# Optimization experiments

Measured on AMD Instinct MI355X. Metric: run time of the kernel, lower is better.

The kernel has to match this reference:

```python
import jax, jax.numpy as jnp
import numpy as np

B, N, K, IN_CH = 512, 64, 16, 6   # graphs, nodes per graph, knn, input features
EPS = 1e-5


def _w(key, shape, fan_in):
    return jax.random.normal(key, shape, jnp.float32) / np.sqrt(fan_in)


def setup_inputs() -> dict:
    key = jax.random.key(0)
    ks = jax.random.split(key, 16)
    f32 = jnp.float32
    inp = {
        "x": jax.random.normal(ks[0], (B * N, IN_CH), f32),
        "batch": (jnp.arange(B * N, dtype=jnp.int32) // N).astype(jnp.int32),
        # input projection 6 -> 64
        "w_in": _w(ks[1], (IN_CH, 64), IN_CH), "g_in": jnp.ones(64, f32), "b_in": jnp.zeros(64, f32),
        # ec1: SharedMLP([128, 64, 64])
        "w1a": _w(ks[2], (128, 64), 128), "g1a": jnp.ones(64, f32), "b1a": jnp.zeros(64, f32),
        "w1b": _w(ks[3], (64, 64), 64),   "g1b": jnp.ones(64, f32), "b1b": jnp.zeros(64, f32),
        # ec2: SharedMLP([128, 128, 128])
        "w2a": _w(ks[4], (128, 128), 128), "g2a": jnp.ones(128, f32), "b2a": jnp.zeros(128, f32),
        "w2b": _w(ks[5], (128, 128), 128), "g2b": jnp.ones(128, f32), "b2b": jnp.zeros(128, f32),
        # ec3: SharedMLP([256, 256, 256])
        "w3a": _w(ks[6], (256, 256), 256), "g3a": jnp.ones(256, f32), "b3a": jnp.zeros(256, f32),
        "w3b": _w(ks[7], (256, 256), 256), "g3b": jnp.ones(256, f32), "b3b": jnp.zeros(256, f32),
        # classifier head (dropout is identity in eval mode)
        "wc1": _w(ks[8], (896, 512), 896), "gc1": jnp.ones(512, f32), "bc1": jnp.zeros(512, f32),
        "wc2": _w(ks[9], (512, 256), 512), "gc2": jnp.ones(256, f32), "bc2": jnp.zeros(256, f32),
        "wc3": _w(ks[10], (256, 2), 256),  "bc3": jnp.zeros(2, f32),
    }
    return inp


def bn(h, g, b):
    # training-mode BatchNorm1d over all leading (node/edge) dims, biased var
    ax = tuple(range(h.ndim - 1))
    m = h.mean(ax)
    v = h.var(ax)
    return g * (h - m) * jax.lax.rsqrt(v + EPS) + b


def lrelu(h):
    return jax.nn.leaky_relu(h, 0.2)


def knn(x):
    # x: [B,N,C]; per-graph squared-Euclidean kNN (excluding self)
    sq = jnp.sum(x * x, -1)
    d = sq[:, :, None] - 2.0 * jnp.einsum('bnc,bmc->bnm', x, x) + sq[:, None, :]
    _, idx = jax.lax.top_k(-d, K + 1)  # K+1 smallest distances
    return idx[:, :, 1:]               # drop self -> [B,N,K]


def edge_conv(x, w1, g1, b1, w2, g2, b2):
    # Dynamic EdgeConv, aggr='max'. Edge (src=centre c, dst=neighbour n):
    # target x_i = x_n, message = MLP(cat[x_i, x_j - x_i]) with x_j = x_c.
    idx = knn(x)                                     # [B,N,K]
    xn = jax.vmap(lambda xb, ib: xb[ib])(x, idx)     # [B,N,K,C] neighbours
    xc = x[:, :, None, :]                            # centres broadcast
    feat = jnp.concatenate([xn, xc - xn], -1)        # [B,N,K,2C]
    h = lrelu(bn(feat @ w1, g1, b1))
    h = lrelu(bn(h @ w2, g2, b2))                    # [B,N,K,Cout]
    C = h.shape[-1]

    def scatter_max(ib, hb):  # per-graph max-scatter to destination nodes
        out = jnp.full((N, C), -jnp.inf, hb.dtype)
        return out.at[ib.reshape(-1)].max(hb.reshape(-1, C))

    res = jax.vmap(scatter_max)(idx, h)
    return jnp.where(jnp.isneginf(res), 0.0, res)    # nodes w/o in-edges -> 0


def reference(x, batch, w_in, g_in, b_in,
              w1a, g1a, b1a, w1b, g1b, b1b,
              w2a, g2a, b2a, w2b, g2b, b2b,
              w3a, g3a, b3a, w3b, g3b, b3b,
              wc1, gc1, bc1, wc2, gc2, bc2, wc3, bc3):
    # batch == arange(B*N)//N (equal-size graphs), encoded by the [B,N] reshape
    h0 = lrelu(bn(x @ w_in, g_in, b_in)).reshape(B, N, 64)
    h1 = edge_conv(h0, w1a, g1a, b1a, w1b, g1b, b1b)   # [B,N,64]
    h2 = edge_conv(h1, w2a, g2a, b2a, w2b, g2b, b2b)   # [B,N,128]
    h3 = edge_conv(h2, w3a, g3a, b3a, w3b, g3b, b3b)   # [B,N,256]
    h = jnp.concatenate([h1, h2, h3], -1)              # [B,N,448]
    pooled = jnp.concatenate([h.mean(1), h.max(1)], -1)  # [B,896]
    z = lrelu(bn(pooled @ wc1, gc1, bc1))
    z = lrelu(bn(z @ wc2, gc2, bc2))
    return z @ wc3 + bc3                               # [B,2] logits
```

## Files before the change

kernel.cpp:

```cpp
#include <hip/hip_runtime.h>
#include <hip/hip_fp16.h>
#include <math.h>

#define BB 512
#define NN 64
#define KNB 16
#define NPTS (BB*NN)
#define NEDGE (BB*NN*KNB)
#define EPSV 1e-5f

typedef __attribute__((ext_vector_type(8))) _Float16 f16x8;
typedef __attribute__((ext_vector_type(4))) _Float16 f16x4;
typedef __attribute__((ext_vector_type(4))) float f32x4;

__device__ __forceinline__ float lrelu(float x){ return x > 0.0f ? x : 0.2f*x; }
__device__ __forceinline__ unsigned encf(float f){
    unsigned u = __float_as_uint(f);
    return (u & 0x80000000u) ? ~u : (u | 0x80000000u);
}
__device__ __forceinline__ float decf(unsigned e){
    unsigned u = (e & 0x80000000u) ? (e ^ 0x80000000u) : ~e;
    return __uint_as_float(u);
}
#define ENC_NEGINF 0x007FFFFFu

__device__ __forceinline__ void split2h(float v, _Float16& h, _Float16& m){
    h = (_Float16)v;
    float r = v - (float)h;
    m = (_Float16)(r * 2048.0f);
}

__global__ void k_input(const float* __restrict__ x, const float* __restrict__ w,
                        float* __restrict__ h0){
    __shared__ float wls[6*64];
    int t = threadIdx.x;
    for (int i = t; i < 6*64; i += 256) wls[i] = w[i];
    __syncthreads();
    int row = blockIdx.x*256 + t;
    float xv[6];
#pragma unroll
    for (int k = 0; k < 6; k++) xv[k] = x[row*6 + k];
#pragma unroll 8
    for (int c = 0; c < 64; c++){
        float acc = 0.f;
#pragma unroll
        for (int k = 0; k < 6; k++) acc += xv[k]*wls[k*64 + c];
        h0[(size_t)row*64 + c] = acc;
    }
}

__global__ void k_colstats_part(const float* __restrict__ h,
                                float* __restrict__ pS, float* __restrict__ pQ){
    int t = threadIdx.x;
    int c = t & 63;
    int g = t >> 6;
    int p = blockIdx.x*4 + g;
    const int rpb = NPTS/256;
    int r0 = p*rpb;
    float s = 0.f, q = 0.f;
    for (int r = r0; r < r0 + rpb; r++){
        float v = h[(size_t)r*64 + c];
        s += v; q += v*v;
    }
    pS[c*256 + p] = s;
    pQ[c*256 + p] = q;
}

__global__ void k_bnfin_part(const float* __restrict__ pS, const float* __restrict__ pQ,
                             const float* __restrict__ g, const float* __restrict__ b,
                             float* __restrict__ cA, float* __restrict__ cB,
                             int P, float invM){
    int c = threadIdx.x;
    const float* ps = pS + (size_t)c*P;
    const float* pq = pQ + (size_t)c*P;
    float s = 0.f, q = 0.f;
    for (int p = 0; p < P; p += 4){
        float4 vs = *(const float4*)(ps + p);
        float4 vq = *(const float4*)(pq + p);
        s += vs.x + vs.y + vs.z + vs.w;
        q += vq.x + vq.y + vq.z + vq.w;
    }
    float m = s*invM;
    float v = q*invM - m*m;
    v = v < 0.f ? 0.f : v;
    float a = g[c]*rsqrtf(v + EPSV);
    cA[c] = a;
    cB[c] = b[c] - m*a;
}

__global__ void k_bnfin(const float* gs, const float* gq, const float* g,
                        const float* b, float* cA, float* cB, int C, float invM){
    int c = blockIdx.x*blockDim.x + threadIdx.x;
    if (c < C){
        float m = gs[c]*invM;
        float v = gq[c]*invM - m*m;
        v = v < 0.f ? 0.f : v;
        float a = g[c]*rsqrtf(v + EPSV);
        cA[c] = a;
        cB[c] = b[c] - m*a;
    }
}

__global__ void k_apply(float* h, const float* __restrict__ cA,
                        const float* __restrict__ cB, int C, int total){
    int i = blockIdx.x*256 + threadIdx.x;
    if (i < total){
        int c = i & (C-1);
        h[i] = lrelu(cA[c]*h[i] + cB[c]);
    }
}

template<int C>
__global__ void k_knn(const float* __restrict__ x, int* __restrict__ idxg){
    const int CP = C + 4;
    __shared__ __align__(16) float xls[64*CP];
    __shared__ float sq[64];
    __shared__ __align__(16) float dls[64*64];
    int t = threadIdx.x, b = blockIdx.x;
    const float* xb = x + (size_t)b*64*C;
    for (int i = t; i < 64*C; i += 256){
        int n = i / C, c = i & (C-1);
        xls[n*CP + c] = xb[i];
    }
    __syncthreads();
    if (t < 64){
        float s = 0.f;
        for (int c = 0; c < C; c += 4){
            float4 v = *(const float4*)&xls[t*CP + c];
            s += v.x*v.x + v.y*v.y + v.z*v.z + v.w*v.w;
        }
        sq[t] = s;
    }
    __syncthreads();
    {
        int n  = t >> 2;
        int m0 = (t & 3)*16;
        float acc[16];
#pragma unroll
        for (int i = 0; i < 16; i++) acc[i] = 0.f;
        const float* an = &xls[n*CP];
        const float* bm = &xls[m0*CP];
        for (int c = 0; c < C; c += 4){
            float4 a = *(const float4*)(an + c);
#pragma unroll
            for (int i = 0; i < 16; i++){
                float4 bv = *(const float4*)(bm + i*CP + c);
                acc[i] += a.x*bv.x + a.y*bv.y + a.z*bv.z + a.w*bv.w;
            }
        }
        float sn = sq[n];
#pragma unroll
        for (int i4 = 0; i4 < 16; i4 += 4){
            float4 dv;
            dv.x = sn - 2.0f*acc[i4+0] + sq[m0+i4+0];
            dv.y = sn - 2.0f*acc[i4+1] + sq[m0+i4+1];
            dv.z = sn - 2.0f*acc[i4+2] + sq[m0+i4+2];
            dv.w = sn - 2.0f*acc[i4+3] + sq[m0+i4+3];
            *(float4*)&dls[n*64 + m0 + i4] = dv;
        }
    }
    __syncthreads();
    int lane = t & 63, w = t >> 6;
    for (int pr = 0; pr < 16; pr += 4){
        int n0 = w*16 + pr;
        unsigned long long c0 = (((unsigned long long)encf(dls[(n0+0)*64 + lane])) << 32) | (unsigned)lane;
        unsigned long long c1 = (((unsigned long long)encf(dls[(n0+1)*64 + lane])) << 32) | (unsigned)lane;
        unsigned long long c2 = (((unsigned long long)encf(dls[(n0+2)*64 + lane])) << 32) | (unsigned)lane;
        unsigned long long c3 = (((unsigned long long)encf(dls[(n0+3)*64 + lane])) << 32) | (unsigned)lane;
#pragma unroll
        for (int k = 2; k <= 64; k <<= 1){
#pragma unroll
            for (int j = k >> 1; j > 0; j >>= 1){
                bool keepmin = ((lane & j) == 0) == ((lane & k) == 0);
                unsigned long long o0 = __shfl_xor(c0, j, 64);
                unsigned long long o1 = __shfl_xor(c1, j, 64);
                unsigned long long o2 = __shfl_xor(c2, j, 64);
                unsigned long long o3 = __shfl_xor(c3, j, 64);
                c0 = keepmin ? (c0 < o0 ? c0 : o0) : (c0 < o0 ? o0 : c0);
                c1 = keepmin ? (c1 < o1 ? c1 : o1) : (c1 < o1 ? o1 : c1);
                c2 = keepmin ? (c2 < o2 ? c2 : o2) : (c2 < o2 ? o2 : c2);
                c3 = keepmin ? (c3 < o3 ? c3 : o3) : (c3 < o3 ? o3 : c3);
            }
        }
        if (lane >= 1 && lane <= KNB){
            int base = b*1024 + n0*16 + lane - 1;
            idxg[base]      = (int)(c0 & 0xffffffffu);
            idxg[base + 16] = (int)(c1 & 0xffffffffu);
            idxg[base + 32] = (int)(c2 & 0xffffffffu);
            idxg[base + 48] = (int)(c3 & 0xffffffffu);
        }
    }
}

template<int CIN, int CMID, bool SPLIT>
__global__ void k_wprep(const float* __restrict__ w1,
                        _Float16* __restrict__ wbh, _Float16* __restrict__ wbm,
                        _Float16* __restrict__ wdh, _Float16* __restrict__ wdm){
    int i = blockIdx.x*256 + threadIdx.x;
    if (i >= CIN*CMID) return;
    int k = i / CMID, c = i - k*CMID;
    float wb = w1[(size_t)(CIN + k)*CMID + c];
    float wd = w1[(size_t)k*CMID + c] - wb;
    size_t o = (size_t)c*CIN + k;
    if (SPLIT){
        _Float16 h, m;
        split2h(wb, h, m); wbh[o] = h; wbm[o] = m;
        split2h(wd, h, m); wdh[o] = h; wdm[o] = m;
    } else {
        wbh[o] = (_Float16)wb;
        wdh[o] = (_Float16)wd;
    }
}

template<int CIN, int CMID>
__global__ __launch_bounds__(256)
void k_mm1x(const float* __restrict__ x,
            const _Float16* __restrict__ wbh, const _Float16* __restrict__ wbm,
            const _Float16* __restrict__ wdh, const _Float16* __restrict__ wdm,
            float* __restrict__ P, float* __restrict__ Q){
    int t = threadIdx.x, b = blockIdx.x;
    int lane = t & 63, w = t >> 6;
    int lrow = lane & 15, lk = lane >> 4;
    const int KT = CIN/32;
    f16x8 ah[KT], am[KT];
    {
        const float* xr = x + ((size_t)b*64 + w*16 + lrow)*CIN;
#pragma unroll
        for (int kt = 0; kt < KT; kt++){
            union { f16x8 v; _Float16 u[8]; } H, M;
#pragma unroll
            for (int j = 0; j < 8; j++)
                split2h(xr[kt*32 + lk*8 + j], H.u[j], M.u[j]);
            ah[kt] = H.v; am[kt] = M.v;
        }
    }
#pragma unroll
    for (int ct = 0; ct < CMID/16; ct++){
        int col = ct*16 + lrow;
        f32x4 aPM = {0,0,0,0}, aPC = {0,0,0,0};
        f32x4 aQM = {0,0,0,0}, aQC = {0,0,0,0};
#pragma unroll
        for (int kt = 0; kt < KT; kt++){
            size_t bo = (size_t)col*CIN + kt*32 + lk*8;
            f16x8 bbh = *(const f16x8*)(wbh + bo);
            f16x8 bbm = *(const f16x8*)(wbm + bo);
            f16x8 bdh = *(const f16x8*)(wdh + bo);
            f16x8 bdm = *(const f16x8*)(wdm + bo);
            aPM = __builtin_amdgcn_mfma_f32_16x16x32_f16(ah[kt], bbh, aPM, 0, 0, 0);
            aPC = __builtin_amdgcn_mfma_f32_16x16x32_f16(ah[kt], bbm, aPC, 0, 0, 0);
            aPC = __builtin_amdgcn_mfma_f32_16x16x32_f16(am[kt], bbh, aPC, 0, 0, 0);
            aQM = __builtin_amdgcn_mfma_f32_16x16x32_f16(ah[kt], bdh, aQM, 0, 0, 0);
            aQC = __builtin_amdgcn_mfma_f32_16x16x32_f16(ah[kt], bdm, aQC, 0, 0, 0);
            aQC = __builtin_amdgcn_mfma_f32_16x16x32_f16(am[kt], bdh, aQC, 0, 0, 0);
        }
#pragma unroll
        for (int u = 0; u < 4; u++){
            size_t o = ((size_t)b*64 + w*16 + lk*4 + u)*CMID + col;
            P[o] = aPM[u] + aPC[u]*(1.0f/2048.0f);
            Q[o] = aQM[u] + aQC[u]*(1.0f/2048.0f);
        }
    }
}

template<int CIN, int CMID>
__global__ __launch_bounds__(256)
void k_mm1xh(const float* __restrict__ x,
             const _Float16* __restrict__ wbh, const _Float16* __restrict__ wdh,
             _Float16* __restrict__ P, _Float16* __restrict__ Q){
    int t = threadIdx.x, b = blockIdx.x;
    int lane = t & 63, w = t >> 6;
    int lrow = lane & 15, lk = lane >> 4;
    const int KT = CIN/32;
    f16x8 ah[KT];
    {
        const float* xr = x + ((size_t)b*64 + w*16 + lrow)*CIN;
#pragma unroll
        for (int kt = 0; kt < KT; kt++){
            union { f16x8 v; _Float16 u[8]; } H;
#pragma unroll
            for (int j = 0; j < 8; j++)
                H.u[j] = (_Float16)xr[kt*32 + lk*8 + j];
            ah[kt] = H.v;
        }
    }
#pragma unroll
    for (int ct = 0; ct < CMID/16; ct++){
        int col = ct*16 + lrow;
        f32x4 aP = {0,0,0,0}, aQ = {0,0,0,0};
#pragma unroll
        for (int kt = 0; kt < KT; kt++){
            size_t bo = (size_t)col*CIN + kt*32 + lk*8;
            f16x8 bbh = *(const f16x8*)(wbh + bo);
            f16x8 bdh = *(const f16x8*)(wdh + bo);
            aP = __builtin_amdgcn_mfma_f32_16x16x32_f16(ah[kt], bbh, aP, 0, 0, 0);
            aQ = __builtin_amdgcn_mfma_f32_16x16x32_f16(ah[kt], bdh, aQ, 0, 0, 0);
        }
#pragma unroll
        for (int u = 0; u < 4; u++){
            size_t o = ((size_t)b*64 + w*16 + lk*4 + u)*CMID + col;
            P[o] = (_Float16)aP[u];
            Q[o] = (_Float16)aQ[u];
        }
    }
}

template<int CMID>
__global__ void k_stats1p(const float* __restrict__ P, const float* __restrict__ Q,
                          const int* __restrict__ idxg,
                          float* __restrict__ pS, float* __restrict__ pQ){
    int t = threadIdx.x, b = blockIdx.x;
    const int NG = 256/CMID;
    const int PT = 512*NG;
    int c = t & (CMID-1);
    int g = t / CMID;
    int epg = 1024/NG;
    const float* Pb = P + (size_t)b*64*CMID;
    const float* Qb = Q + (size_t)b*64*CMID;
    const int* ib = idxg + b*1024;
    float s = 0.f, q = 0.f;
    for (int e = g*epg; e < (g+1)*epg; e++){
        int n = e >> 4;
        int j = ib[e];
        float v = Pb[n*CMID + c] + Qb[j*CMID + c];
        s += v; q += v*v;
    }
    int p = b*NG + g;
    pS[(size_t)c*PT + p] = s;
    pQ[(size_t)c*PT + p] = q;
}

__global__ void k_stats1h(const _Float16* __restrict__ P, const _Float16* __restrict__ Q,
                          const int* __restrict__ idxg,
                          float* __restrict__ pS, float* __restrict__ pQ){
    __shared__ int ils[1024];
    int t = threadIdx.x, b = blockIdx.x;
    for (int i = t; i < 1024; i += 256) ils[i] = idxg[b*1024 + i];
    __syncthreads();
    const _Float16* Pb = P + (size_t)b*64*256;
    const _Float16* Qb = Q + (size_t)b*64*256;
    float s = 0.f, q = 0.f;
    for (int n = 0; n < 64; n++){
        float p = (float)Pb[n*256 + t];
#pragma unroll 4
        for (int k = 0; k < 16; k++){
            int j = ils[n*16 + k];
            float v = p + (float)Qb[j*256 + t];
            s += v; q += v*v;
        }
    }
    pS[(size_t)t*512 + b] = s;
    pQ[(size_t)t*512 + b] = q;
}

template<int CMID, int COUT, int NSET>
__global__ __launch_bounds__(256)
void k_mm2s(const float* __restrict__ P, const float* __restrict__ Q,
            const int* __restrict__ idxg,
            const float* __restrict__ cA1, const float* __restrict__ cB1,
            const float* __restrict__ w2, const float* __restrict__ g2,
            unsigned* __restrict__ outenc,
            float* __restrict__ pS, float* __restrict__ pQ){
    const int AS = CMID + 8;
    const int NCOL = 64*NSET;
    __shared__ __align__(16) _Float16 act_h[32*AS];
    __shared__ __align__(16) _Float16 act_m[32*AS];
    __shared__ unsigned maxtab[NCOL*65];
    __shared__ int ils[1024];
    __shared__ __align__(16) float a1ls[CMID];
    __shared__ __align__(16) float b1ls[CMID];
    int t = threadIdx.x, b = blockIdx.x, cc = blockIdx.y;
    int lane = t & 63, w = t >> 6;
    int lrow = lane & 15, lk = lane >> 4;

    for (int i = t; i < 1024; i += 256) ils[i] = idxg[b*1024 + i];
    for (int i = t; i < CMID; i += 256){ a1ls[i] = cA1[i]; b1ls[i] = cB1[i]; }
    for (int i = t; i < NCOL*65; i += 256) maxtab[i] = ENC_NEGINF;

    const int KT = CMID/32;
    f16x8 bh[NSET][KT], bm[NSET][KT];
    float sg[NSET];
    int ccBase = cc*NCOL;
#pragma unroll
    for (int s = 0; s < NSET; s++){
        int ncol = ccBase + s*64 + w*16 + lrow;
#pragma unroll
        for (int kt = 0; kt < KT; kt++){
            union { f16x8 v; _Float16 u[8]; } uh, um;
#pragma unroll
            for (int j = 0; j < 8; j++){
                int k = kt*32 + lk*8 + j;
                split2h(w2[(size_t)k*COUT + ncol], uh.u[j], um.u[j]);
            }
            bh[s][kt] = uh.v; bm[s][kt] = um.v;
        }
        sg[s] = (g2[ncol] < 0.0f) ? -1.0f : 1.0f;
    }
    float ss[NSET], qq[NSET];
#pragma unroll
    for (int s = 0; s < NSET; s++){ ss[s] = 0.f; qq[s] = 0.f; }
    const float* Pb = P + (size_t)b*64*CMID;
    const float* Qb = Q + (size_t)b*64*CMID;
    __syncthreads();

    for (int ch = 0; ch < 32; ch++){
        for (int i = t*4; i < 32*CMID; i += 1024){
            int le = i / CMID, k = i & (CMID-1);
            int e = ch*32 + le;
            int n = e >> 4, j = ils[e];
            float4 pv = *(const float4*)(Pb + n*CMID + k);
            float4 qv = *(const float4*)(Qb + j*CMID + k);
            float4 ca = *(const float4*)&a1ls[k];
            float4 cb = *(const float4*)&b1ls[k];
            float v0 = lrelu(ca.x*(pv.x + qv.x) + cb.x);
            float v1 = lrelu(ca.y*(pv.y + qv.y) + cb.y);
            float v2 = lrelu(ca.z*(pv.z + qv.z) + cb.z);
            float v3 = lrelu(ca.w*(pv.w + qv.w) + cb.w);
            union { f16x4 v; _Float16 u[4]; } hh, mm;
            split2h(v0, hh.u[0], mm.u[0]);
            split2h(v1, hh.u[1], mm.u[1]);
            split2h(v2, hh.u[2], mm.u[2]);
            split2h(v3, hh.u[3], mm.u[3]);
            *(f16x4*)&act_h[le*AS + k] = hh.v;
            *(f16x4*)&act_m[le*AS + k] = mm.v;
        }
        __syncthreads();

        f32x4 accM[2][NSET], accC[2][NSET];
#pragma unroll
        for (int r = 0; r < 2; r++)
#pragma unroll
            for (int s = 0; s < NSET; s++){
                accM[r][s] = {0.f,0.f,0.f,0.f};
                accC[r][s] = {0.f,0.f,0.f,0.f};
            }
#pragma unroll
        for (int kt = 0; kt < KT; kt++){
            int ko = kt*32 + lk*8;
#pragma unroll
            for (int r = 0; r < 2; r++){
                f16x8 ah = *(const f16x8*)&act_h[(r*16 + lrow)*AS + ko];
                f16x8 am = *(const f16x8*)&act_m[(r*16 + lrow)*AS + ko];
#pragma unroll
                for (int s = 0; s < NSET; s++){
                    accM[r][s] = __builtin_amdgcn_mfma_f32_16x16x32_f16(ah, bh[s][kt], accM[r][s], 0, 0, 0);
                    accC[r][s] = __builtin_amdgcn_mfma_f32_16x16x32_f16(ah, bm[s][kt], accC[r][s], 0, 0, 0);
                    accC[r][s] = __builtin_amdgcn_mfma_f32_16x16x32_f16(am, bh[s][kt], accC[r][s], 0, 0, 0);
                }
            }
        }
#pragma unroll
        for (int r = 0; r < 2; r++){
#pragma unroll
            for (int s = 0; s < NSET; s++){
#pragma unroll
                for (int u = 0; u < 4; u++){
                    int e = ch*32 + r*16 + lk*4 + u;
                    float v = accM[r][s][u] + accC[r][s][u]*(1.0f/2048.0f);
                    ss[s] += v; qq[s] += v*v;
                    int colL = s*64 + w*16 + lrow;
                    atomicMax(&maxtab[colL*65 + ils[e]], encf(sg[s]*v));
                }
            }
        }
        __syncthreads();
    }
#pragma unroll
    for (int s = 0; s < NSET; s++){
        ss[s] += __shfl_xor(ss[s], 16, 64); ss[s] += __shfl_xor(ss[s], 32, 64);
        qq[s] += __shfl_xor(qq[s], 16, 64); qq[s] += __shfl_xor(qq[s], 32, 64);
        if (lane < 16){
            pS[(size_t)(ccBase + s*64 + w*16 + lane)*512 + b] = ss[s];
            pQ[(size_t)(ccBase + s*64 + w*16 + lane)*512 + b] = qq[s];
        }
    }
    for (int i = t; i < 64*NCOL; i += 256){
        int colL = i % NCOL, j = i / NCOL;
        outenc[((size_t)b*64 + j)*COUT + ccBase + colL] = maxtab[colL*65 + j];
    }
}

template<int CMID, int COUT, int NSET>
__global__ __launch_bounds__(256)
void k_mm2xh(const _Float16* __restrict__ P, const _Float16* __restrict__ Q,
             const int* __restrict__ idxg,
             const float* __restrict__ cA1, const float* __restrict__ cB1,
             const float* __restrict__ w2, const float* __restrict__ g2,
             unsigned* __restrict__ outenc,
             float* __restrict__ pS, float* __restrict__ pQ){
    const int AS = CMID + 8;
    const int NCOL = 64*NSET;
    __shared__ __align__(16) _Float16 act[32*AS];
    __shared__ unsigned maxtab[NCOL*65];
    __shared__ int ils[1024];
    __shared__ __align__(16) _Float16 a1h[CMID];
    __shared__ __align__(16) _Float16 b1h[CMID];
    int t = threadIdx.x, b = blockIdx.x, cc = blockIdx.y;
    int lane = t & 63, w = t >> 6;
    int lrow = lane & 15, lk = lane >> 4;

    for (int i = t; i < 1024; i += 256) ils[i] = idxg[b*1024 + i];
    for (int i = t; i < CMID; i += 256){
        a1h[i] = (_Float16)cA1[i];
        b1h[i] = (_Float16)cB1[i];
    }
    for (int i = t; i < NCOL*65; i += 256) maxtab[i] = ENC_NEGINF;

    const int KT = CMID/32;
    f16x8 breg[NSET][KT];
    float sg[NSET];
    int ccBase = cc*NCOL;
#pragma unroll
    for (int s = 0; s < NSET; s++){
        int ncol = ccBase + s*64 + w*16 + lrow;
#pragma unroll
        for (int kt = 0; kt < KT; kt++){
            union { f16x8 v; _Float16 u[8]; } bu;
#pragma unroll
            for (int j = 0; j < 8; j++){
                int k = kt*32 + lk*8 + j;
                bu.u[j] = (_Float16)w2[(size_t)k*COUT + ncol];
            }
            breg[s][kt] = bu.v;
        }
        sg[s] = (g2[ncol] < 0.0f) ? -1.0f : 1.0f;
    }
    float ss[NSET], qq[NSET];
#pragma unroll
    for (int s = 0; s < NSET; s++){ ss[s] = 0.f; qq[s] = 0.f; }
    const _Float16* Pb = P + (size_t)b*64*CMID;
    const _Float16* Qb = Q + (size_t)b*64*CMID;
    __syncthreads();

    for (int ch = 0; ch < 32; ch++){
        for (int i = t*8; i < 32*CMID; i += 2048){
            int le = i / CMID, k = i & (CMID-1);
            int e = ch*32 + le;
            int n = e >> 4, j = ils[e];
            f16x8 pv = *(const f16x8*)(Pb + (size_t)n*CMID + k);
            f16x8 qv = *(const f16x8*)(Qb + (size_t)j*CMID + k);
            f16x8 ca = *(const f16x8*)&a1h[k];
            f16x8 cb = *(const f16x8*)&b1h[k];
            f16x8 v = ca*(pv + qv) + cb;
            f16x8 vm = v * (_Float16)0.2f;
            union { f16x8 x; _Float16 e8[8]; } V, M, R;
            V.x = v; M.x = vm;
#pragma unroll
            for (int u = 0; u < 8; u++)
                R.e8[u] = (V.e8[u] > (_Float16)0.0f) ? V.e8[u] : M.e8[u];
            *(f16x8*)&act[le*AS + k] = R.x;
        }
        __syncthreads();

        f32x4 acc[2][NSET];
#pragma unroll
        for (int r = 0; r < 2; r++)
#pragma unroll
            for (int s = 0; s < NSET; s++) acc[r][s] = {0.f,0.f,0.f,0.f};
#pragma unroll
        for (int kt = 0; kt < KT; kt++){
            int ko = kt*32 + lk*8;
#pragma unroll
            for (int r = 0; r < 2; r++){
                f16x8 a = *(const f16x8*)&act[(r*16 + lrow)*AS + ko];
#pragma unroll
                for (int s = 0; s < NSET; s++)
                    acc[r][s] = __builtin_amdgcn_mfma_f32_16x16x32_f16(a, breg[s][kt], acc[r][s], 0, 0, 0);
            }
        }
#pragma unroll
        for (int r = 0; r < 2; r++){
#pragma unroll
            for (int s = 0; s < NSET; s++){
#pragma unroll
                for (int u = 0; u < 4; u++){
                    int e = ch*32 + r*16 + lk*4 + u;
                    float v = acc[r][s][u];
                    ss[s] += v; qq[s] += v*v;
                    int colL = s*64 + w*16 + lrow;
                    atomicMax(&maxtab[colL*65 + ils[e]], encf(sg[s]*v));
                }
            }
        }
        __syncthreads();
    }
#pragma unroll
    for (int s = 0; s < NSET; s++){
        ss[s] += __shfl_xor(ss[s], 16, 64); ss[s] += __shfl_xor(ss[s], 32, 64);
        qq[s] += __shfl_xor(qq[s], 16, 64); qq[s] += __shfl_xor(qq[s], 32, 64);
        if (lane < 16){
            pS[(size_t)(ccBase + s*64 + w*16 + lane)*512 + b] = ss[s];
            pQ[(size_t)(ccBase + s*64 + w*16 + lane)*512 + b] = qq[s];
        }
    }
    for (int i = t; i < 64*NCOL; i += 256){
        int colL = i % NCOL, j = i / NCOL;
        outenc[((size_t)b*64 + j)*COUT + ccBase + colL] = maxtab[colL*65 + j];
    }
}

__global__ void k_final_ec(unsigned* __restrict__ buf, const float* __restrict__ cA,
                           const float* __restrict__ cB, const float* __restrict__ g,
                           int C, int total){
    int i = blockIdx.x*256 + threadIdx.x;
    if (i >= total) return;
    int c = i & (C-1);
    unsigned e = buf[i];
    float r;
    if (e == ENC_NEGINF) r = 0.0f;
    else {
        float s = (g[c] < 0.0f) ? -1.0f : 1.0f;
        float v = s*decf(e);
        r = lrelu(cA[c]*v + cB[c]);
    }
    ((float*)buf)[i] = r;
}

__global__ void k_pool(const float* __restrict__ h1, const float* __restrict__ h2,
                       const unsigned* __restrict__ h3e,
                       const float* __restrict__ cA3, const float* __restrict__ cB3,
                       const float* __restrict__ g3, float* __restrict__ pooled){
    int t = threadIdx.x, b = blockIdx.x;
    for (int c = t; c < 448; c += 256){
        float s = 0.f, mx = -INFINITY;
        if (c < 192){
            const float* src; int C, cl;
            if (c < 64){ src = h1; C = 64;  cl = c; }
            else { src = h2; C = 128; cl = c - 64; }
            const float* p = src + (size_t)b*64*C + cl;
            for (int n = 0; n < 64; n++){
                float v = p[(size_t)n*C];
                s += v; mx = fmaxf(mx, v);
            }
        } else {
            int cl = c - 192;
            float ca = cA3[cl], cb = cB3[cl];
            float sgn = (g3[cl] < 0.0f) ? -1.0f : 1.0f;
            const unsigned* p = h3e + (size_t)b*64*256 + cl;
            for (int n = 0; n < 64; n++){
                unsigned e = p[(size_t)n*256];
                float v;
                if (e == ENC_NEGINF) v = 0.0f;
                else v = lrelu(ca*(sgn*decf(e)) + cb);
                s += v; mx = fmaxf(mx, v);
            }
        }
        pooled[b*896 + c] = s*(1.0f/64.0f);
        pooled[b*896 + 448 + c] = mx;
    }
}

__global__ void k_fc1(const float* __restrict__ pooled, const float* __restrict__ w,
                      float* __restrict__ z, float* gs, float* gq){
    int r = blockIdx.x;
    int co = blockIdx.y*256 + threadIdx.x;
    const float* pr = pooled + r*896;
    float acc = 0.f;
    for (int k = 0; k < 896; k++) acc += pr[k]*w[(size_t)k*512 + co];
    z[(size_t)r*512 + co] = acc;
    atomicAdd(&gs[co], acc);
    atomicAdd(&gq[co], acc*acc);
}

__global__ void k_fc2(const float* __restrict__ z1, const float* __restrict__ cA,
                      const float* __restrict__ cB, const float* __restrict__ w,
                      float* __restrict__ z2, float* gs, float* gq){
    int r = blockIdx.x;
    int co = threadIdx.x;
    const float* zr = z1 + (size_t)r*512;
    float acc = 0.f;
    for (int k = 0; k < 512; k++){
        float v = lrelu(cA[k]*zr[k] + cB[k]);
        acc += v*w[(size_t)k*256 + co];
    }
    z2[(size_t)r*256 + co] = acc;
    atomicAdd(&gs[co], acc);
    atomicAdd(&gq[co], acc*acc);
}

__global__ void k_fc3(const float* __restrict__ z2, const float* __restrict__ cA,
                      const float* __restrict__ cB, const float* __restrict__ w,
                      const float* __restrict__ bias, float* __restrict__ out){
    int r = blockIdx.x*256 + threadIdx.x;
    const float* zr = z2 + (size_t)r*256;
    float a0 = 0.f, a1 = 0.f;
    for (int k = 0; k < 256; k++){
        float v = lrelu(cA[k]*zr[k] + cB[k]);
        a0 += v*w[k*2 + 0];
        a1 += v*w[k*2 + 1];
    }
    out[r*2 + 0] = a0 + bias[0];
    out[r*2 + 1] = a1 + bias[1];
}

extern "C" void kernel_launch(void* const* d_in, const int* in_sizes, int n_in,
                              void* d_out, int out_size, void* d_ws, size_t ws_size,
                              hipStream_t stream){
    const float* x    = (const float*)d_in[0];
    const float* w_in = (const float*)d_in[2];
    const float* g_in = (const float*)d_in[3];
    const float* b_in = (const float*)d_in[4];
    const float* w1a  = (const float*)d_in[5];
    const float* g1a  = (const float*)d_in[6];
    const float* b1a  = (const float*)d_in[7];
    const float* w1b  = (const float*)d_in[8];
    const float* g1b  = (const float*)d_in[9];
    const float* b1b  = (const float*)d_in[10];
    const float* w2a  = (const float*)d_in[11];
    const float* g2a  = (const float*)d_in[12];
    const float* b2a  = (const float*)d_in[13];
    const float* w2b  = (const float*)d_in[14];
    const float* g2b  = (const float*)d_in[15];
    const float* b2b  = (const float*)d_in[16];
    const float* w3a  = (const float*)d_in[17];
    const float* g3a  = (const float*)d_in[18];
    const float* b3a  = (const float*)d_in[19];
    const float* w3b  = (const float*)d_in[20];
    const float* g3b  = (const float*)d_in[21];
    const float* b3b  = (const float*)d_in[22];
    const float* wc1  = (const float*)d_in[23];
    const float* gc1  = (const float*)d_in[24];
    const float* bc1  = (const float*)d_in[25];
    const float* wc2  = (const float*)d_in[26];
    const float* gc2  = (const float*)d_in[27];
    const float* bc2  = (const float*)d_in[28];
    const float* wc3  = (const float*)d_in[29];
    const float* bc3  = (const float*)d_in[30];

    char* ws = (char*)d_ws;
    size_t off = 0;
    auto alloc = [&](size_t bytes){
        size_t o = off; off = (off + bytes + 255) & ~(size_t)255; return o;
    };
    float* h0     = (float*)(ws + alloc((size_t)NPTS*64*4));
    float* h1     = (float*)(ws + alloc((size_t)NPTS*64*4));
    float* h2     = (float*)(ws + alloc((size_t)NPTS*128*4));
    float* h3     = (float*)(ws + alloc((size_t)NPTS*256*4));
    float* P      = (float*)(ws + alloc((size_t)NPTS*256*4));
    float* Q      = (float*)(ws + alloc((size_t)NPTS*256*4));
    int*   idx    = (int*)  (ws + alloc((size_t)NPTS*16*4));
    float* pooled = (float*)(ws + alloc((size_t)512*896*4));
    float* z1     = (float*)(ws + alloc((size_t)512*512*4));
    float* z2     = (float*)(ws + alloc((size_t)512*256*4));
    float* pS     = (float*)(ws + alloc((size_t)131072*4));
    float* pQ     = (float*)(ws + alloc((size_t)131072*4));
    float* stats  = (float*)(ws + alloc((size_t)2048*4));
    float* coefs  = (float*)(ws + alloc((size_t)3456*4));
    _Float16* wsp = (_Float16*)(ws + alloc((size_t)114688*2));

    _Float16 *w1bh = wsp,          *w1bm = wsp+4096,
             *w1dh = wsp+8192,     *w1dm = wsp+12288;
    _Float16 *w2bh = wsp+16384,    *w2bm = wsp+24576,
             *w2dh = wsp+32768,    *w2dm = wsp+40960;
    _Float16 *w3bh = wsp+49152,    *w3dh = wsp+81920;

    float *f1s  = stats,       *f1q  = stats+512;
    float *f2s  = stats+1024,  *f2q  = stats+1280;
    float *cA0   = coefs,      *cB0   = coefs+64;
    float *cA1a  = coefs+128,  *cB1a  = coefs+192;
    float *cA1b  = coefs+256,  *cB1b  = coefs+320;
    float *cA2a  = coefs+384,  *cB2a  = coefs+512;
    float *cA2b  = coefs+640,  *cB2b  = coefs+768;
    float *cA3a  = coefs+896,  *cB3a  = coefs+1152;
    float *cA3b  = coefs+1408, *cB3b  = coefs+1664;
    float *cAf1  = coefs+1920, *cBf1  = coefs+2432;
    float *cAf2  = coefs+2944, *cBf2  = coefs+3200;

    (void)hipMemsetAsync(stats, 0, 2048*4, stream);

    k_wprep<64,64,true><<<16, 256, 0, stream>>>(w1a, w1bh, w1bm, w1dh, w1dm);
    k_wprep<64,128,true><<<32, 256, 0, stream>>>(w2a, w2bh, w2bm, w2dh, w2dm);
    k_wprep<128,256,false><<<128, 256, 0, stream>>>(w3a, w3bh, nullptr, w3dh, nullptr);

    k_input<<<NPTS/256, 256, 0, stream>>>(x, w_in, h0);
    k_colstats_part<<<64, 256, 0, stream>>>(h0, pS, pQ);
    k_bnfin_part<<<1, 64, 0, stream>>>(pS, pQ, g_in, b_in, cA0, cB0, 256, 1.0f/NPTS);
    k_apply<<<(NPTS*64)/256, 256, 0, stream>>>(h0, cA0, cB0, 64, NPTS*64);

    k_knn<64><<<BB, 256, 0, stream>>>(h0, idx);
    k_mm1x<64,64><<<BB, 256, 0, stream>>>(h0, w1bh, w1bm, w1dh, w1dm, P, Q);
    k_stats1p<64><<<BB, 256, 0, stream>>>(P, Q, idx, pS, pQ);
    k_bnfin_part<<<1, 64, 0, stream>>>(pS, pQ, g1a, b1a, cA1a, cB1a, 2048, 1.0f/NEDGE);
    k_mm2s<64,64,1><<<dim3(BB,1), 256, 0, stream>>>(P, Q, idx, cA1a, cB1a, w1b, g1b,
                                                    (unsigned*)h1, pS, pQ);
    k_bnfin_part<<<1, 64, 0, stream>>>(pS, pQ, g1b, b1b, cA1b, cB1b, 512, 1.0f/NEDGE);
    k_final_ec<<<(NPTS*64)/256, 256, 0, stream>>>((unsigned*)h1, cA1b, cB1b, g1b, 64, NPTS*64);

    k_knn<64><<<BB, 256, 0, stream>>>(h1, idx);
    k_mm1x<64,128><<<BB, 256, 0, stream>>>(h1, w2bh, w2bm, w2dh, w2dm, P, Q);
    k_stats1p<128><<<BB, 256, 0, stream>>>(P, Q, idx, pS, pQ);
    k_bnfin_part<<<1, 128, 0, stream>>>(pS, pQ, g2a, b2a, cA2a, cB2a, 1024, 1.0f/NEDGE);
    k_mm2s<128,128,2><<<dim3(BB,1), 256, 0, stream>>>(P, Q, idx, cA2a, cB2a, w2b, g2b,
                                                      (unsigned*)h2, pS, pQ);
    k_bnfin_part<<<1, 128, 0, stream>>>(pS, pQ, g2b, b2b, cA2b, cB2b, 512, 1.0f/NEDGE);
    k_final_ec<<<(NPTS*128)/256, 256, 0, stream>>>((unsigned*)h2, cA2b, cB2b, g2b, 128, NPTS*128);

    k_knn<128><<<BB, 256, 0, stream>>>(h2, idx);
    k_mm1xh<128,256><<<BB, 256, 0, stream>>>(h2, w3bh, w3dh, (_Float16*)P, (_Float16*)Q);
    k_stats1h<<<BB, 256, 0, stream>>>((_Float16*)P, (_Float16*)Q, idx, pS, pQ);
    k_bnfin_part<<<1, 256, 0, stream>>>(pS, pQ, g3a, b3a, cA3a, cB3a, 512, 1.0f/NEDGE);
    k_mm2xh<256,256,2><<<dim3(BB,2), 256, 0, stream>>>((_Float16*)P, (_Float16*)Q, idx,
                                                       cA3a, cB3a, w3b, g3b,
                                                       (unsigned*)h3, pS, pQ);
    k_bnfin_part<<<1, 256, 0, stream>>>(pS, pQ, g3b, b3b, cA3b, cB3b, 512, 1.0f/NEDGE);

    k_pool<<<BB, 256, 0, stream>>>(h1, h2, (const unsigned*)h3, cA3b, cB3b, g3b, pooled);
    k_fc1<<<dim3(512,2), 256, 0, stream>>>(pooled, wc1, z1, f1s, f1q);
    k_bnfin<<<2, 256, 0, stream>>>(f1s, f1q, gc1, bc1, cAf1, cBf1, 512, 1.0f/512);
    k_fc2<<<512, 256, 0, stream>>>(z1, cAf1, cBf1, wc2, z2, f2s, f2q);
    k_bnfin<<<1, 256, 0, stream>>>(f2s, f2q, gc2, bc2, cAf2, cBf2, 256, 1.0f/512);
    k_fc3<<<2, 256, 0, stream>>>(z2, cAf2, cBf2, wc3, bc3, (float*)d_out);

    (void)in_sizes; (void)n_in; (void)out_size; (void)ws_size;
}
```

Before: 1.243 ms.

## Prefetch next chunk's gathered P/Q into registers and shrink shared index table

In both edge-MLP second-layer kernels, the P/Q gather loads for the next 32-edge chunk are issued into registers right after the barrier, so global latency overlaps the MFMA and atomic-max work of the current chunk. The neighbour index table is stored as bytes in shared memory, and the BN scale/shift constants are held in registers instead of shared arrays. Launch bounds now request 3 blocks per SM, and lrelu becomes an fmax. Extra prefetch registers combined with the tighter occupancy bound may cause register spills.

```diff
diff --git a/kernel.cpp b/kernel.cpp
--- a/kernel.cpp
+++ b/kernel.cpp
@@ -13,7 +13,7 @@
 typedef __attribute__((ext_vector_type(4))) _Float16 f16x4;
 typedef __attribute__((ext_vector_type(4))) float f32x4;
 
-__device__ __forceinline__ float lrelu(float x){ return x > 0.0f ? x : 0.2f*x; }
+__device__ __forceinline__ float lrelu(float x){ return fmaxf(x, 0.2f*x); }
 __device__ __forceinline__ unsigned encf(float f){
     unsigned u = __float_as_uint(f);
     return (u & 0x80000000u) ? ~u : (u | 0x80000000u);
@@ -353,7 +353,7 @@
 }
 
 template<int CMID, int COUT, int NSET>
-__global__ __launch_bounds__(256)
+__global__ __launch_bounds__(256, 3)
 void k_mm2s(const float* __restrict__ P, const float* __restrict__ Q,
             const int* __restrict__ idxg,
             const float* __restrict__ cA1, const float* __restrict__ cB1,
@@ -362,19 +362,23 @@
             float* __restrict__ pS, float* __restrict__ pQ){
     const int AS = CMID + 8;
     const int NCOL = 64*NSET;
+    const int NM = CMID/32;
+    const int LESTEP = 1024/CMID;
     __shared__ __align__(16) _Float16 act_h[32*AS];
     __shared__ __align__(16) _Float16 act_m[32*AS];
     __shared__ unsigned maxtab[NCOL*65];
-    __shared__ int ils[1024];
-    __shared__ __align__(16) float a1ls[CMID];
-    __shared__ __align__(16) float b1ls[CMID];
+    __shared__ unsigned char ils8[1024];
     int t = threadIdx.x, b = blockIdx.x, cc = blockIdx.y;
     int lane = t & 63, w = t >> 6;
     int lrow = lane & 15, lk = lane >> 4;
 
-    for (int i = t; i < 1024; i += 256) ils[i] = idxg[b*1024 + i];
-    for (int i = t; i < CMID; i += 256){ a1ls[i] = cA1[i]; b1ls[i] = cB1[i]; }
+    for (int i = t; i < 1024; i += 256) ils8[i] = (unsigned char)idxg[b*1024 + i];
     for (int i = t; i < NCOL*65; i += 256) maxtab[i] = ENC_NEGINF;
+
+    int kq  = (t*4) & (CMID-1);
+    int le0 = (t*4) / CMID;
+    float4 caq = *(const float4*)(cA1 + kq);
+    float4 cbq = *(const float4*)(cB1 + kq);
 
     const int KT = CMID/32;
     f16x8 bh[NSET][KT], bm[NSET][KT];
@@ -402,28 +406,49 @@
     const float* Qb = Q + (size_t)b*64*CMID;
     __syncthreads();
 
+    float4 pvr[NM], qvr[NM];
+#pragma unroll
+    for (int m = 0; m < NM; m++){
+        int le = le0 + LESTEP*m;
+        int j = ils8[le];
+        pvr[m] = *(const float4*)(Pb + (le >> 4)*CMID + kq);
+        qvr[m] = *(const float4*)(Qb + (size_t)j*CMID + kq);
+    }
+
     for (int ch = 0; ch < 32; ch++){
-        for (int i = t*4; i < 32*CMID; i += 1024){
-            int le = i / CMID, k = i & (CMID-1);
-            int e = ch*32 + le;
-            int n = e >> 4, j = ils[e];
-            float4 pv = *(const float4*)(Pb + n*CMID + k);
-            float4 qv = *(const float4*)(Qb + j*CMID + k);
-            float4 ca = *(const float4*)&a1ls[k];
-            float4 cb = *(const float4*)&b1ls[k];
-            float v0 = lrelu(ca.x*(pv.x + qv.x) + cb.x);
-            float v1 = lrelu(ca.y*(pv.y + qv.y) + cb.y);
-            float v2 = lrelu(ca.z*(pv.z + qv.z) + cb.z);
-            float v3 = lrelu(ca.w*(pv.w + qv.w) + cb.w);
+#pragma unroll
+        for (int m = 0; m < NM; m++){
+            int le = le0 + LESTEP*m;
+            float4 pv = pvr[m], qv = qvr[m];
+            float v0 = lrelu(caq.x*(pv.x + qv.x) + cbq.x);
+            float v1 = lrelu(caq.y*(pv.y + qv.y) + cbq.y);
+            float v2 = lrelu(caq.z*(pv.z + qv.z) + cbq.z);
+            float v3 = lrelu(caq.w*(pv.w + qv.w) + cbq.w);
             union { f16x4 v; _Float16 u[4]; } hh, mm;
             split2h(v0, hh.u[0], mm.u[0]);
             split2h(v1, hh.u[1], mm.u[1]);
             split2h(v2, hh.u[2], mm.u[2]);
             split2h(v3, hh.u[3], mm.u[3]);
-            *(f16x4*)&act_h[le*AS + k] = hh.v;
-            *(f16x4*)&act_m[le*AS + k] = mm.v;
+            *(f16x4*)&act_h[le*AS + kq] = hh.v;
+            *(f16x4*)&act_m[le*AS + kq] = mm.v;
         }
         __syncthreads();
+
+        if (ch < 31){
+#pragma unroll
+            for (int m = 0; m < NM; m++){
+                int le = le0 + LESTEP*m;
+                int j = ils8[(ch+1)*32 + le];
+                pvr[m] = *(const float4*)(Pb + ((ch+1)*2 + (le >> 4))*CMID + kq);
+                qvr[m] = *(const float4*)(Qb + (size_t)j*CMID + kq);
+            }
+        }
+        int jj[2][4];
+#pragma unroll
+        for (int r = 0; r < 2; r++)
+#pragma unroll
+            for (int u = 0; u < 4; u++)
+                jj[r][u] = ils8[ch*32 + r*16 + lk*4 + u];
 
         f32x4 accM[2][NSET], accC[2][NSET];
 #pragma unroll
@@ -454,11 +479,10 @@
             for (int s = 0; s < NSET; s++){
 #pragma unroll
                 for (int u = 0; u < 4; u++){
-                    int e = ch*32 + r*16 + lk*4 + u;
                     float v = accM[r][s][u] + accC[r][s][u]*(1.0f/2048.0f);
                     ss[s] += v; qq[s] += v*v;
                     int colL = s*64 + w*16 + lrow;
-                    atomicMax(&maxtab[colL*65 + ils[e]], encf(sg[s]*v));
+                    atomicMax(&maxtab[colL*65 + jj[r][u]], encf(sg[s]*v));
                 }
             }
         }
@@ -480,7 +504,7 @@
 }
 
 template<int CMID, int COUT, int NSET>
-__global__ __launch_bounds__(256)
+__global__ __launch_bounds__(256, 3)
 void k_mm2xh(const _Float16* __restrict__ P, const _Float16* __restrict__ Q,
              const int* __restrict__ idxg,
              const float* __restrict__ cA1, const float* __restrict__ cB1,
@@ -489,21 +513,26 @@
              float* __restrict__ pS, float* __restrict__ pQ){
     const int AS = CMID + 8;
     const int NCOL = 64*NSET;
+    const int NM = CMID/64;
+    const int LESTEP = 2048/CMID;
     __shared__ __align__(16) _Float16 act[32*AS];
     __shared__ unsigned maxtab[NCOL*65];
-    __shared__ int ils[1024];
-    __shared__ __align__(16) _Float16 a1h[CMID];
-    __shared__ __align__(16) _Float16 b1h[CMID];
+    __shared__ unsigned char ils8[1024];
     int t = threadIdx.x, b = blockIdx.x, cc = blockIdx.y;
     int lane = t & 63, w = t >> 6;
     int lrow = lane & 15, lk = lane >> 4;
 
-    for (int i = t; i < 1024; i += 256) ils[i] = idxg[b*1024 + i];
-    for (int i = t; i < CMID; i += 256){
-        a1h[i] = (_Float16)cA1[i];
-        b1h[i] = (_Float16)cB1[i];
-    }
+    for (int i = t; i < 1024; i += 256) ils8[i] = (unsigned char)idxg[b*1024 + i];
     for (int i = t; i < NCOL*65; i += 256) maxtab[i] = ENC_NEGINF;
+
+    int kq  = (t*8) & (CMID-1);
+    int le0 = (t*8) / CMID;
+    union { f16x8 v; _Float16 u[8]; } cah, cbh;
+#pragma unroll
+    for (int j = 0; j < 8; j++){
+        cah.u[j] = (_Float16)cA1[kq + j];
+        cbh.u[j] = (_Float16)cB1[kq + j];
+    }
 
     const int KT = CMID/32;
     f16x8 breg[NSET][KT];
@@ -531,25 +560,45 @@
     const _Float16* Qb = Q + (size_t)b*64*CMID;
     __syncthreads();
 
+    f16x8 pvr[NM], qvr[NM];
+#pragma unroll
+    for (int m = 0; m < NM; m++){
+        int le = le0 + LESTEP*m;
+        int j = ils8[le];
+        pvr[m] = *(const f16x8*)(Pb + (size_t)(le >> 4)*CMID + kq);
+        qvr[m] = *(const f16x8*)(Qb + (size_t)j*CMID + kq);
+    }
+
     for (int ch = 0; ch < 32; ch++){
-        for (int i = t*8; i < 32*CMID; i += 2048){
-            int le = i / CMID, k = i & (CMID-1);
-            int e = ch*32 + le;
-            int n = e >> 4, j = ils[e];
-            f16x8 pv = *(const f16x8*)(Pb + (size_t)n*CMID + k);
-            f16x8 qv = *(const f16x8*)(Qb + (size_t)j*CMID + k);
-            f16x8 ca = *(const f16x8*)&a1h[k];
-            f16x8 cb = *(const f16x8*)&b1h[k];
-            f16x8 v = ca*(pv + qv) + cb;
+#pragma unroll
+        for (int m = 0; m < NM; m++){
+            int le = le0 + LESTEP*m;
+            f16x8 v = cah.v*(pvr[m] + qvr[m]) + cbh.v;
             f16x8 vm = v * (_Float16)0.2f;
             union { f16x8 x; _Float16 e8[8]; } V, M, R;
             V.x = v; M.x = vm;
 #pragma unroll
             for (int u = 0; u < 8; u++)
                 R.e8[u] = (V.e8[u] > (_Float16)0.0f) ? V.e8[u] : M.e8[u];
-            *(f16x8*)&act[le*AS + k] = R.x;
+            *(f16x8*)&act[le*AS + kq] = R.x;
         }
         __syncthreads();
+
+        if (ch < 31){
+#pragma unroll
+            for (int m = 0; m < NM; m++){
+                int le = le0 + LESTEP*m;
+                int j = ils8[(ch+1)*32 + le];
+                pvr[m] = *(const f16x8*)(Pb + (size_t)((ch+1)*2 + (le >> 4))*CMID + kq);
+                qvr[m] = *(const f16x8*)(Qb + (size_t)j*CMID + kq);
+            }
+        }
+        int jj[2][4];
+#pragma unroll
+        for (int r = 0; r < 2; r++)
+#pragma unroll
+            for (int u = 0; u < 4; u++)
+                jj[r][u] = ils8[ch*32 + r*16 + lk*4 + u];
 
         f32x4 acc[2][NSET];
 #pragma unroll
@@ -573,11 +622,10 @@
             for (int s = 0; s < NSET; s++){
 #pragma unroll
                 for (int u = 0; u < 4; u++){
-                    int e = ch*32 + r*16 + lk*4 + u;
                     float v = acc[r][s][u];
                     ss[s] += v; qq[s] += v*v;
                     int colL = s*64 + w*16 + lrow;
-                    atomicMax(&maxtab[colL*65 + ils[e]], encf(sg[s]*v));
+                    atomicMax(&maxtab[colL*65 + jj[r][u]], encf(sg[s]*v));
                 }
             }
         }
```

Measured after the change: 1.179 ms. 5.2% less time.
